# Kernel optimization log

Hardware: AMD Instinct MI355X
Metric: run time of the kernel (lower is better)

Reference implementation:

```python
import jax, jax.numpy as jnp
import numpy as np

NUM_EXPERTS = 32
TOP_K = 4
HIDDEN = 1024
FFN = 2048
BATCH, SEQ = 1, 1024


def setup_inputs() -> dict:
    key = jax.random.key(0)
    ks = jax.random.split(key, 4)
    s = 0.02
    return {
        "x": jax.random.normal(ks[0], (BATCH, SEQ, HIDDEN), jnp.float32),
        "gate_w": jax.random.normal(ks[1], (HIDDEN, NUM_EXPERTS), jnp.float32) * s,
        "gate_b": jnp.zeros((NUM_EXPERTS,), jnp.float32),
        "w1": jax.random.normal(ks[2], (NUM_EXPERTS, HIDDEN, FFN), jnp.float32) * s,
        "b1": jnp.zeros((NUM_EXPERTS, FFN), jnp.float32),
        "w2": jax.random.normal(ks[3], (NUM_EXPERTS, FFN, HIDDEN), jnp.float32) * s,
        "b2": jnp.zeros((NUM_EXPERTS, HIDDEN), jnp.float32),
        "load_ema": jnp.ones((NUM_EXPERTS,), jnp.float32) / NUM_EXPERTS,
        "top_k": TOP_K,
    }


def reference(x, gate_w, gate_b, w1, b1, w2, b2, load_ema, top_k):
    # x: [B, S, d]; eval-mode CompoundMoELayer forward.
    B, S, d = x.shape
    E = gate_w.shape[1]
    flat = x.reshape(-1, d)                              # [N, d]
    N = flat.shape[0]

    # --- router: gate logits -> top-k -> softmax over selected logits ---
    logits = flat @ gate_w + gate_b                      # [N, E]
    top_vals, top_idx = jax.lax.top_k(logits, top_k)     # [N, k]
    weights = jax.nn.softmax(top_vals, axis=-1)          # [N, k]

    # --- switch-style load-balance aux loss ---
    probs = jax.nn.softmax(logits, axis=-1)              # [N, E]
    counts = jax.nn.one_hot(top_idx, E, dtype=flat.dtype).sum(axis=1)  # [N, E]
    frac = counts.mean(axis=0) / top_k                   # [E] routed fraction
    base_aux = E * jnp.sum(frac * probs.mean(axis=0))

    # --- dense combine weights [N, E]: zero for non-selected experts ---
    comb = jnp.zeros((N, E), flat.dtype).at[jnp.arange(N)[:, None], top_idx].add(weights)

    # --- per-expert FFN (GELU, exact erf as torch default), combined ---
    def step(acc, p):
        W1, bb1, W2, bb2, ce = p                         # ce: [N] combine weight
        h = jax.nn.gelu(flat @ W1 + bb1, approximate=False)
        y = h @ W2 + bb2
        return acc + ce[:, None] * y, None

    out, _ = jax.lax.scan(step, jnp.zeros_like(flat), (w1, b1, w2, b2, comb.T))

    # --- compound entropy regularizer over expert load EMA buffer ---
    lp = load_ema / (load_ema.sum() + 1e-8)
    entropy = -jnp.sum(lp * jnp.log(lp + 1e-8))
    reg = jnp.log(jnp.asarray(E, flat.dtype)) - entropy
    aux = base_aux + 0.001 * reg
    return out.reshape(B, S, d), aux
```

## Files before the change

kernel.cpp:

```cpp
#include <hip/hip_runtime.h>
#include <hip/hip_bf16.h>
#include <cmath>

#define N_TOK 1024
#define DIM   1024
#define FFN   2048
#define NE    32
#define TOPK  4
#define TM    256
#define TN    64
#define BK    32
#define BS_STRIDE 40

typedef __attribute__((ext_vector_type(8))) short bf16x8;
typedef __attribute__((ext_vector_type(4))) float f32x4;

#define GLOBAL_AS __attribute__((address_space(1)))
#define LDS_AS    __attribute__((address_space(3)))

__device__ __forceinline__ void g2lds16(const void* g, void* l) {
    __builtin_amdgcn_global_load_lds((const GLOBAL_AS void*)g, (LDS_AS void*)l, 16, 0, 0);
}

__global__ void router_kernel(const float* __restrict__ x, const float* __restrict__ gw,
                              const float* __restrict__ gb, float* __restrict__ probs_mat,
                              int* __restrict__ top_idx, float* __restrict__ top_w) {
    __shared__ float part[8][32];
    __shared__ float logit_s[32];
    int t = threadIdx.x;
    int token = blockIdx.x;
    int e = t & 31, p = t >> 5;
    const float* xr = x + (size_t)token * DIM;
    float acc = 0.f;
    int i0 = p * (DIM / 8);
    for (int i = 0; i < DIM / 8; ++i)
        acc += xr[i0 + i] * gw[(size_t)(i0 + i) * NE + e];
    part[p][e] = acc;
    __syncthreads();
    if (t < 32) {
        float l = gb[t];
        for (int q = 0; q < 8; ++q) l += part[q][t];
        logit_s[t] = l;
    }
    __syncthreads();
    if (t == 0) {
        float l[32];
        for (int i = 0; i < 32; ++i) l[i] = logit_s[i];
        float m = -1e30f;
        for (int i = 0; i < 32; ++i) m = fmaxf(m, l[i]);
        float denom = 0.f;
        for (int i = 0; i < 32; ++i) denom += expf(l[i] - m);
        for (int i = 0; i < 32; ++i)
            probs_mat[(size_t)token * 32 + i] = expf(l[i] - m) / denom;
        float lc[32];
        for (int i = 0; i < 32; ++i) lc[i] = l[i];
        int idx[TOPK]; float val[TOPK];
        for (int k = 0; k < TOPK; ++k) {
            int bj = 0; float bv = lc[0];
            for (int i = 1; i < 32; ++i) if (lc[i] > bv) { bv = lc[i]; bj = i; }
            idx[k] = bj; val[k] = bv; lc[bj] = -1e30f;
        }
        float mm = val[0];
        float w[TOPK]; float ss = 0.f;
        for (int k = 0; k < TOPK; ++k) { w[k] = expf(val[k] - mm); ss += w[k]; }
        for (int k = 0; k < TOPK; ++k) {
            top_idx[token * TOPK + k] = idx[k];
            top_w[token * TOPK + k] = w[k] / ss;
        }
    }
}

__global__ void aux_kernel(const float* __restrict__ probs_mat, const int* __restrict__ top_idx,
                           const float* __restrict__ load_ema, int* __restrict__ counts,
                           int* __restrict__ offsets, int* __restrict__ cursors,
                           float* __restrict__ out_aux) {
    __shared__ int cnt_s[32];
    __shared__ float ps[32];
    __shared__ float psum_part[8][32];
    int t = threadIdx.x;
    if (t < 32) cnt_s[t] = 0;
    __syncthreads();
    for (int i = t; i < N_TOK * TOPK; i += 256) atomicAdd(&cnt_s[top_idx[i]], 1);
    int e = t & 31, p = t >> 5;
    float s = 0.f;
    for (int tok = p; tok < N_TOK; tok += 8) s += probs_mat[(size_t)tok * 32 + e];
    psum_part[p][e] = s;
    __syncthreads();
    if (t < 32) {
        float tot = 0.f;
        for (int q = 0; q < 8; ++q) tot += psum_part[q][t];
        ps[t] = tot;
        counts[t] = cnt_s[t];
    }
    __syncthreads();
    if (t == 0) {
        int off = 0;
        for (int i = 0; i < 32; ++i) { offsets[i] = off; cursors[i] = off; off += cnt_s[i]; }
        offsets[32] = off;
        float base = 0.f;
        for (int i = 0; i < 32; ++i) {
            float frac = (float)cnt_s[i] / (float)(N_TOK * TOPK);
            float mp = ps[i] / (float)N_TOK;
            base += frac * mp;
        }
        base *= (float)NE;
        float sum_ema = 0.f;
        for (int i = 0; i < 32; ++i) sum_ema += load_ema[i];
        float H = 0.f;
        for (int i = 0; i < 32; ++i) {
            float lp = load_ema[i] / (sum_ema + 1e-8f);
            H -= lp * logf(lp + 1e-8f);
        }
        float reg = logf((float)NE) - H;
        *out_aux = base + 0.001f * reg;
    }
}

__global__ void scatter_kernel(const int* __restrict__ top_idx, int* __restrict__ cursors,
                               int* __restrict__ pair_token, int* __restrict__ pair_of) {
    int token = blockIdx.x * 256 + threadIdx.x;
    if (token >= N_TOK) return;
    for (int s = 0; s < TOPK; ++s) {
        int e = top_idx[token * TOPK + s];
        int pos = atomicAdd(&cursors[e], 1);
        pair_token[pos] = token;
        pair_of[token * TOPK + s] = pos;
    }
}

__global__ void convert_x_kernel(const float* __restrict__ x, __hip_bfloat16* __restrict__ xb) {
    int i = (blockIdx.x * 256 + threadIdx.x) * 4;
    float4 v = *(const float4*)&x[i];
    union { __hip_bfloat16 h[4]; ushort4 u; } pk;
    pk.h[0] = __float2bfloat16(v.x);
    pk.h[1] = __float2bfloat16(v.y);
    pk.h[2] = __float2bfloat16(v.z);
    pk.h[3] = __float2bfloat16(v.w);
    *(ushort4*)&xb[i] = pk.u;
}

__global__ __launch_bounds__(256) void gemm1_kernel(
        const __hip_bfloat16* __restrict__ xb, const float* __restrict__ w1,
        const float* __restrict__ b1, const int* __restrict__ offsets,
        const int* __restrict__ pair_token, __hip_bfloat16* __restrict__ h) {
    int e = blockIdx.z;
    int m0 = offsets[e], Me = offsets[e + 1] - m0;
    int rowBase = blockIdx.y * TM;
    if (rowBase >= Me) return;
    int mlim = Me - rowBase; if (mlim > TM) mlim = TM;
    int f0 = blockIdx.x * TN;

    __shared__ __hip_bfloat16 As[TM * BK];
    __shared__ __hip_bfloat16 Bs[TN * BS_STRIDE];
    __shared__ int toks[TM];

    int t = threadIdx.x;
    int w = t >> 6, ln = t & 63;
    int q = ln >> 4, lj = ln & 15;
    { int r = t < mlim ? t : mlim - 1; toks[t] = pair_token[m0 + rowBase + r]; }
    bool act = (w * 64) < mlim;

    int a_sub = ln >> 2, a_part = ln & 3;
    int bn = ln, bkb = w * 8;

    f32x4 acc[4][4] = {};

    for (int k0 = 0; k0 < DIM; k0 += BK) {
        __syncthreads();
        if (act) {
#pragma unroll
            for (int i = 0; i < 4; ++i) {
                int rit = w * 64 + i * 16 + a_sub;
                const __hip_bfloat16* src = xb + (size_t)toks[rit] * DIM + k0 + a_part * 8;
                g2lds16(src, As + (w * 64 + i * 16) * BK);
            }
        }
        {
            const float* bp = w1 + ((size_t)e * DIM + k0 + bkb) * FFN + f0 + bn;
            float bv[8];
#pragma unroll
            for (int j = 0; j < 8; ++j) bv[j] = bp[(size_t)j * FFN];
            union { __hip_bfloat16 hb[8]; int4 v; } u;
#pragma unroll
            for (int j = 0; j < 8; ++j) u.hb[j] = __float2bfloat16(bv[j]);
            *(int4*)&Bs[bn * BS_STRIDE + bkb] = u.v;
        }
        __syncthreads();
        if (act) {
            bf16x8 af[4], bf[4];
#pragma unroll
            for (int ms = 0; ms < 4; ++ms)
                af[ms] = *(const bf16x8*)&As[(w * 64 + ms * 16 + lj) * BK + q * 8];
#pragma unroll
            for (int ns = 0; ns < 4; ++ns)
                bf[ns] = *(const bf16x8*)&Bs[(ns * 16 + lj) * BS_STRIDE + q * 8];
#pragma unroll
            for (int ms = 0; ms < 4; ++ms)
#pragma unroll
                for (int ns = 0; ns < 4; ++ns)
                    acc[ms][ns] = __builtin_amdgcn_mfma_f32_16x16x32_bf16(af[ms], bf[ns], acc[ms][ns], 0, 0, 0);
        }
    }
    if (!act) return;
#pragma unroll
    for (int ms = 0; ms < 4; ++ms) {
#pragma unroll
        for (int rr = 0; rr < 4; ++rr) {
            int rit = w * 64 + ms * 16 + q * 4 + rr;
            if (rit >= mlim) continue;
            size_t rowG = (size_t)(m0 + rowBase + rit);
#pragma unroll
            for (int ns = 0; ns < 4; ++ns) {
                int col = f0 + ns * 16 + lj;
                float v = acc[ms][ns][rr] + b1[(size_t)e * FFN + col];
                float g = 0.5f * v * (1.f + erff(v * 0.70710678118654752f));
                h[rowG * FFN + col] = __float2bfloat16(g);
            }
        }
    }
}

__global__ __launch_bounds__(256) void gemm2_kernel(
        const __hip_bfloat16* __restrict__ h, const float* __restrict__ w2,
        const int* __restrict__ offsets, float* __restrict__ y) {
    int e = blockIdx.z;
    int m0 = offsets[e], Me = offsets[e + 1] - m0;
    int rowBase = blockIdx.y * TM;
    if (rowBase >= Me) return;
    int mlim = Me - rowBase; if (mlim > TM) mlim = TM;
    int d0 = blockIdx.x * TN;

    __shared__ __hip_bfloat16 As[TM * BK];
    __shared__ __hip_bfloat16 Bs[TN * BS_STRIDE];

    int t = threadIdx.x;
    int w = t >> 6, ln = t & 63;
    int q = ln >> 4, lj = ln & 15;
    bool act = (w * 64) < mlim;

    int a_sub = ln >> 2, a_part = ln & 3;
    int bn = ln, bkb = w * 8;

    f32x4 acc[4][4] = {};

    for (int k0 = 0; k0 < FFN; k0 += BK) {
        __syncthreads();
        if (act) {
#pragma unroll
            for (int i = 0; i < 4; ++i) {
                int rit = w * 64 + i * 16 + a_sub;
                if (rit >= mlim) rit = mlim - 1;
                const __hip_bfloat16* src = h + (size_t)(m0 + rowBase + rit) * FFN + k0 + a_part * 8;
                g2lds16(src, As + (w * 64 + i * 16) * BK);
            }
        }
        {
            const float* bp = w2 + ((size_t)e * FFN + k0 + bkb) * DIM + d0 + bn;
            float bv[8];
#pragma unroll
            for (int j = 0; j < 8; ++j) bv[j] = bp[(size_t)j * DIM];
            union { __hip_bfloat16 hb[8]; int4 v; } u;
#pragma unroll
            for (int j = 0; j < 8; ++j) u.hb[j] = __float2bfloat16(bv[j]);
            *(int4*)&Bs[bn * BS_STRIDE + bkb] = u.v;
        }
        __syncthreads();
        if (act) {
            bf16x8 af[4], bf[4];
#pragma unroll
            for (int ms = 0; ms < 4; ++ms)
                af[ms] = *(const bf16x8*)&As[(w * 64 + ms * 16 + lj) * BK + q * 8];
#pragma unroll
            for (int ns = 0; ns < 4; ++ns)
                bf[ns] = *(const bf16x8*)&Bs[(ns * 16 + lj) * BS_STRIDE + q * 8];
#pragma unroll
            for (int ms = 0; ms < 4; ++ms)
#pragma unroll
                for (int ns = 0; ns < 4; ++ns)
                    acc[ms][ns] = __builtin_amdgcn_mfma_f32_16x16x32_bf16(af[ms], bf[ns], acc[ms][ns], 0, 0, 0);
        }
    }
    if (!act) return;
#pragma unroll
    for (int ms = 0; ms < 4; ++ms) {
#pragma unroll
        for (int rr = 0; rr < 4; ++rr) {
            int rit = w * 64 + ms * 16 + q * 4 + rr;
            if (rit >= mlim) continue;
            size_t rowG = (size_t)(m0 + rowBase + rit);
#pragma unroll
            for (int ns = 0; ns < 4; ++ns)
                y[rowG * DIM + d0 + ns * 16 + lj] = acc[ms][ns][rr];
        }
    }
}

__global__ void combine_kernel(const float* __restrict__ y, const float* __restrict__ b2,
        const int* __restrict__ top_idx, const float* __restrict__ top_w,
        const int* __restrict__ pair_of, float* __restrict__ out) {
    int token = blockIdx.y;
    int j = blockIdx.x * 256 + threadIdx.x;
    float acc = 0.f;
#pragma unroll
    for (int s = 0; s < TOPK; ++s) {
        int e = top_idx[token * TOPK + s];
        float w = top_w[token * TOPK + s];
        int p = pair_of[token * TOPK + s];
        acc += w * (y[(size_t)p * DIM + j] + b2[(size_t)e * DIM + j]);
    }
    out[(size_t)token * DIM + j] = acc;
}

extern "C" void kernel_launch(void* const* d_in, const int* in_sizes, int n_in,
                              void* d_out, int out_size, void* d_ws, size_t ws_size,
                              hipStream_t stream) {
    const float* x        = (const float*)d_in[0];
    const float* gate_w   = (const float*)d_in[1];
    const float* gate_b   = (const float*)d_in[2];
    const float* w1       = (const float*)d_in[3];
    const float* b1       = (const float*)d_in[4];
    const float* w2       = (const float*)d_in[5];
    const float* b2       = (const float*)d_in[6];
    const float* load_ema = (const float*)d_in[7];
    float* out = (float*)d_out;

    char* base = (char*)d_ws;
    size_t off = 0;
    auto alloc = [&](size_t bytes) {
        void* p = base + off;
        off = (off + bytes + 255) & ~(size_t)255;
        return p;
    };
    float* probs_mat = (float*)alloc(N_TOK * 32 * sizeof(float));
    int*   top_idx   = (int*)  alloc(N_TOK * TOPK * sizeof(int));
    float* top_w     = (float*)alloc(N_TOK * TOPK * sizeof(float));
    int*   counts    = (int*)  alloc(32 * sizeof(int));
    int*   offsets   = (int*)  alloc(33 * sizeof(int));
    int*   cursors   = (int*)  alloc(32 * sizeof(int));
    int*   pair_token= (int*)  alloc(N_TOK * TOPK * sizeof(int));
    int*   pair_of   = (int*)  alloc(N_TOK * TOPK * sizeof(int));
    __hip_bfloat16* xb = (__hip_bfloat16*)alloc((size_t)N_TOK * DIM * sizeof(__hip_bfloat16));
    __hip_bfloat16* h  = (__hip_bfloat16*)alloc((size_t)N_TOK * TOPK * FFN * sizeof(__hip_bfloat16));
    float* y         = (float*)alloc((size_t)N_TOK * TOPK * DIM * sizeof(float));

    router_kernel<<<N_TOK, 256, 0, stream>>>(x, gate_w, gate_b, probs_mat, top_idx, top_w);
    aux_kernel<<<1, 256, 0, stream>>>(probs_mat, top_idx, load_ema, counts, offsets, cursors,
                                      out + (size_t)N_TOK * DIM);
    scatter_kernel<<<(N_TOK + 255) / 256, 256, 0, stream>>>(top_idx, cursors, pair_token, pair_of);
    convert_x_kernel<<<(N_TOK * DIM / 4 + 255) / 256, 256, 0, stream>>>(x, xb);
    {
        dim3 grid(FFN / TN, (N_TOK * 1 + TM - 1) / TM, NE);
        gemm1_kernel<<<grid, 256, 0, stream>>>(xb, w1, b1, offsets, pair_token, h);
    }
    {
        dim3 grid(DIM / TN, (N_TOK * 1 + TM - 1) / TM, NE);
        gemm2_kernel<<<grid, 256, 0, stream>>>(h, w2, offsets, y);
    }
    {
        dim3 grid(DIM / 256, N_TOK);
        combine_kernel<<<grid, 256, 0, stream>>>(y, b2, top_idx, top_w, pair_of, out);
    }
}
```

Before: 759.3 us.

## Loop row tiles inside expert GEMM blocks, split-K gemm2, fuse x convert into router

GEMM blocks now iterate over all row tiles of an expert instead of launching one block per tile, with TM reduced to 192 and a transposed LDS layout for A. gemm2 splits the FFN reduction in two, writing two partial outputs that the combine kernel sums. The bf16 conversion of x is folded into the router, and router softmax/top-k use wave shuffles instead of a single thread. This aims to cut empty blocks, launch count and serial router work, at the cost of per-expert load imbalance and extra y traffic.

```diff
diff --git a/kernel.cpp b/kernel.cpp
--- a/kernel.cpp
+++ b/kernel.cpp
@@ -7,7 +7,7 @@
 #define FFN   2048
 #define NE    32
 #define TOPK  4
-#define TM    256
+#define TM    192
 #define TN    64
 #define BK    32
 #define BS_STRIDE 40
@@ -22,58 +22,66 @@
     __builtin_amdgcn_global_load_lds((const GLOBAL_AS void*)g, (LDS_AS void*)l, 16, 0, 0);
 }
 
-__global__ void router_kernel(const float* __restrict__ x, const float* __restrict__ gw,
-                              const float* __restrict__ gb, float* __restrict__ probs_mat,
-                              int* __restrict__ top_idx, float* __restrict__ top_w) {
+__global__ __launch_bounds__(256) void router_kernel(
+        const float* __restrict__ x, const float* __restrict__ gw,
+        const float* __restrict__ gb, float* __restrict__ probs_mat,
+        int* __restrict__ top_idx, float* __restrict__ top_w,
+        __hip_bfloat16* __restrict__ xb) {
     __shared__ float part[8][32];
     __shared__ float logit_s[32];
     int t = threadIdx.x;
     int token = blockIdx.x;
+    const float* xr = x + (size_t)token * DIM;
+    {
+        float4 v = *(const float4*)&xr[t * 4];
+        union { __hip_bfloat16 h[4]; ushort4 u; } pk;
+        pk.h[0] = __float2bfloat16(v.x); pk.h[1] = __float2bfloat16(v.y);
+        pk.h[2] = __float2bfloat16(v.z); pk.h[3] = __float2bfloat16(v.w);
+        *(ushort4*)&xb[(size_t)token * DIM + t * 4] = pk.u;
+    }
     int e = t & 31, p = t >> 5;
-    const float* xr = x + (size_t)token * DIM;
     float acc = 0.f;
     int i0 = p * (DIM / 8);
     for (int i = 0; i < DIM / 8; ++i)
         acc += xr[i0 + i] * gw[(size_t)(i0 + i) * NE + e];
     part[p][e] = acc;
     __syncthreads();
-    if (t < 32) {
-        float l = gb[t];
-        for (int q = 0; q < 8; ++q) l += part[q][t];
-        logit_s[t] = l;
-    }
-    __syncthreads();
-    if (t == 0) {
-        float l[32];
-        for (int i = 0; i < 32; ++i) l[i] = logit_s[i];
-        float m = -1e30f;
-        for (int i = 0; i < 32; ++i) m = fmaxf(m, l[i]);
-        float denom = 0.f;
-        for (int i = 0; i < 32; ++i) denom += expf(l[i] - m);
-        for (int i = 0; i < 32; ++i)
-            probs_mat[(size_t)token * 32 + i] = expf(l[i] - m) / denom;
-        float lc[32];
-        for (int i = 0; i < 32; ++i) lc[i] = l[i];
-        int idx[TOPK]; float val[TOPK];
-        for (int k = 0; k < TOPK; ++k) {
-            int bj = 0; float bv = lc[0];
-            for (int i = 1; i < 32; ++i) if (lc[i] > bv) { bv = lc[i]; bj = i; }
-            idx[k] = bj; val[k] = bv; lc[bj] = -1e30f;
-        }
-        float mm = val[0];
-        float w[TOPK]; float ss = 0.f;
-        for (int k = 0; k < TOPK; ++k) { w[k] = expf(val[k] - mm); ss += w[k]; }
-        for (int k = 0; k < TOPK; ++k) {
-            top_idx[token * TOPK + k] = idx[k];
-            top_w[token * TOPK + k] = w[k] / ss;
+    if (t < 64) {
+        float l = -3e38f;
+        if (t < 32) {
+            l = gb[t];
+            for (int q = 0; q < 8; ++q) l += part[q][t];
+        }
+        float m = l;
+        for (int off = 32; off >= 1; off >>= 1) m = fmaxf(m, __shfl_xor(m, off, 64));
+        float ex = (t < 32) ? expf(l - m) : 0.f;
+        float den = ex;
+        for (int off = 32; off >= 1; off >>= 1) den += __shfl_xor(den, off, 64);
+        if (t < 32) probs_mat[(size_t)token * 32 + t] = ex / den;
+        float v = l;
+        float vals[TOPK]; int idxs[TOPK];
+        for (int r = 0; r < TOPK; ++r) {
+            float mv = v;
+            for (int off = 32; off >= 1; off >>= 1) mv = fmaxf(mv, __shfl_xor(mv, off, 64));
+            unsigned long long mask = __ballot(v == mv);
+            int idx = __ffsll((unsigned long long)(mask & 0xffffffffull)) - 1;
+            vals[r] = mv; idxs[r] = idx;
+            if (t == idx) v = -3e38f;
+        }
+        if (t == 0) {
+            float w[TOPK]; float ss = 0.f;
+            for (int r = 0; r < TOPK; ++r) { w[r] = expf(vals[r] - vals[0]); ss += w[r]; }
+            for (int r = 0; r < TOPK; ++r) {
+                top_idx[token * TOPK + r] = idxs[r];
+                top_w[token * TOPK + r] = w[r] / ss;
+            }
         }
     }
 }
 
 __global__ void aux_kernel(const float* __restrict__ probs_mat, const int* __restrict__ top_idx,
-                           const float* __restrict__ load_ema, int* __restrict__ counts,
-                           int* __restrict__ offsets, int* __restrict__ cursors,
-                           float* __restrict__ out_aux) {
+                           const float* __restrict__ load_ema, int* __restrict__ offsets,
+                           int* __restrict__ cursors, float* __restrict__ out_aux) {
     __shared__ int cnt_s[32];
     __shared__ float ps[32];
     __shared__ float psum_part[8][32];
@@ -90,7 +98,6 @@
         float tot = 0.f;
         for (int q = 0; q < 8; ++q) tot += psum_part[q][t];
         ps[t] = tot;
-        counts[t] = cnt_s[t];
     }
     __syncthreads();
     if (t == 0) {
@@ -100,8 +107,7 @@
         float base = 0.f;
         for (int i = 0; i < 32; ++i) {
             float frac = (float)cnt_s[i] / (float)(N_TOK * TOPK);
-            float mp = ps[i] / (float)N_TOK;
-            base += frac * mp;
+            base += frac * (ps[i] / (float)N_TOK);
         }
         base *= (float)NE;
         float sum_ema = 0.f;
@@ -111,8 +117,7 @@
             float lp = load_ema[i] / (sum_ema + 1e-8f);
             H -= lp * logf(lp + 1e-8f);
         }
-        float reg = logf((float)NE) - H;
-        *out_aux = base + 0.001f * reg;
+        *out_aux = base + 0.001f * (logf((float)NE) - H);
     }
 }
 
@@ -128,169 +133,141 @@
     }
 }
 
-__global__ void convert_x_kernel(const float* __restrict__ x, __hip_bfloat16* __restrict__ xb) {
-    int i = (blockIdx.x * 256 + threadIdx.x) * 4;
-    float4 v = *(const float4*)&x[i];
-    union { __hip_bfloat16 h[4]; ushort4 u; } pk;
-    pk.h[0] = __float2bfloat16(v.x);
-    pk.h[1] = __float2bfloat16(v.y);
-    pk.h[2] = __float2bfloat16(v.z);
-    pk.h[3] = __float2bfloat16(v.w);
-    *(ushort4*)&xb[i] = pk.u;
-}
-
-__global__ __launch_bounds__(256) void gemm1_kernel(
+__global__ __launch_bounds__(256, 4) void gemm1_kernel(
         const __hip_bfloat16* __restrict__ xb, const float* __restrict__ w1,
         const float* __restrict__ b1, const int* __restrict__ offsets,
         const int* __restrict__ pair_token, __hip_bfloat16* __restrict__ h) {
     int e = blockIdx.z;
     int m0 = offsets[e], Me = offsets[e + 1] - m0;
-    int rowBase = blockIdx.y * TM;
-    if (rowBase >= Me) return;
-    int mlim = Me - rowBase; if (mlim > TM) mlim = TM;
     int f0 = blockIdx.x * TN;
 
-    __shared__ __hip_bfloat16 As[TM * BK];
+    __shared__ short As[4 * TM * 8];
     __shared__ __hip_bfloat16 Bs[TN * BS_STRIDE];
     __shared__ int toks[TM];
 
     int t = threadIdx.x;
     int w = t >> 6, ln = t & 63;
     int q = ln >> 4, lj = ln & 15;
-    { int r = t < mlim ? t : mlim - 1; toks[t] = pair_token[m0 + rowBase + r]; }
-    bool act = (w * 64) < mlim;
-
-    int a_sub = ln >> 2, a_part = ln & 3;
     int bn = ln, bkb = w * 8;
 
-    f32x4 acc[4][4] = {};
-
-    for (int k0 = 0; k0 < DIM; k0 += BK) {
-        __syncthreads();
-        if (act) {
-#pragma unroll
-            for (int i = 0; i < 4; ++i) {
-                int rit = w * 64 + i * 16 + a_sub;
-                const __hip_bfloat16* src = xb + (size_t)toks[rit] * DIM + k0 + a_part * 8;
-                g2lds16(src, As + (w * 64 + i * 16) * BK);
-            }
-        }
-        {
-            const float* bp = w1 + ((size_t)e * DIM + k0 + bkb) * FFN + f0 + bn;
-            float bv[8];
-#pragma unroll
-            for (int j = 0; j < 8; ++j) bv[j] = bp[(size_t)j * FFN];
-            union { __hip_bfloat16 hb[8]; int4 v; } u;
-#pragma unroll
-            for (int j = 0; j < 8; ++j) u.hb[j] = __float2bfloat16(bv[j]);
-            *(int4*)&Bs[bn * BS_STRIDE + bkb] = u.v;
-        }
-        __syncthreads();
-        if (act) {
-            bf16x8 af[4], bf[4];
-#pragma unroll
-            for (int ms = 0; ms < 4; ++ms)
-                af[ms] = *(const bf16x8*)&As[(w * 64 + ms * 16 + lj) * BK + q * 8];
+    float bias[4];
+#pragma unroll
+    for (int ns = 0; ns < 4; ++ns) bias[ns] = b1[(size_t)e * FFN + f0 + ns * 16 + lj];
+
+    for (int mb = 0; mb < Me; mb += TM) {
+        int mlim = Me - mb; if (mlim > TM) mlim = TM;
+        if (t < TM) {
+            int r = t < mlim ? t : mlim - 1;
+            toks[t] = pair_token[m0 + mb + r];
+        }
+        f32x4 acc[3][4] = {};
+        for (int k0 = 0; k0 < DIM; k0 += BK) {
+            __syncthreads();
+#pragma unroll
+            for (int c = 0; c < 3; ++c) {
+                const __hip_bfloat16* src = xb + (size_t)toks[c * 64 + ln] * DIM + k0 + w * 8;
+                g2lds16(src, As + (w * TM + c * 64) * 8);
+            }
+            {
+                const float* bp = w1 + ((size_t)e * DIM + k0 + bkb) * FFN + f0 + bn;
+                union { __hip_bfloat16 hb[8]; int4 v; } u;
+#pragma unroll
+                for (int j = 0; j < 8; ++j) u.hb[j] = __float2bfloat16(bp[(size_t)j * FFN]);
+                *(int4*)&Bs[bn * BS_STRIDE + bkb] = u.v;
+            }
+            __syncthreads();
+            bf16x8 af[3], bf[4];
+#pragma unroll
+            for (int ms = 0; ms < 3; ++ms)
+                af[ms] = *(const bf16x8*)&As[(q * TM + w * 48 + ms * 16 + lj) * 8];
 #pragma unroll
             for (int ns = 0; ns < 4; ++ns)
                 bf[ns] = *(const bf16x8*)&Bs[(ns * 16 + lj) * BS_STRIDE + q * 8];
 #pragma unroll
-            for (int ms = 0; ms < 4; ++ms)
+            for (int ms = 0; ms < 3; ++ms)
 #pragma unroll
                 for (int ns = 0; ns < 4; ++ns)
                     acc[ms][ns] = __builtin_amdgcn_mfma_f32_16x16x32_bf16(af[ms], bf[ns], acc[ms][ns], 0, 0, 0);
         }
-    }
-    if (!act) return;
-#pragma unroll
-    for (int ms = 0; ms < 4; ++ms) {
-#pragma unroll
-        for (int rr = 0; rr < 4; ++rr) {
-            int rit = w * 64 + ms * 16 + q * 4 + rr;
-            if (rit >= mlim) continue;
-            size_t rowG = (size_t)(m0 + rowBase + rit);
-#pragma unroll
-            for (int ns = 0; ns < 4; ++ns) {
-                int col = f0 + ns * 16 + lj;
-                float v = acc[ms][ns][rr] + b1[(size_t)e * FFN + col];
-                float g = 0.5f * v * (1.f + erff(v * 0.70710678118654752f));
-                h[rowG * FFN + col] = __float2bfloat16(g);
-            }
-        }
-    }
-}
-
-__global__ __launch_bounds__(256) void gemm2_kernel(
+#pragma unroll
+        for (int ms = 0; ms < 3; ++ms) {
+#pragma unroll
+            for (int rr = 0; rr < 4; ++rr) {
+                int rit = w * 48 + ms * 16 + q * 4 + rr;
+                if (rit >= mlim) continue;
+                size_t rowG = (size_t)(m0 + mb + rit);
+#pragma unroll
+                for (int ns = 0; ns < 4; ++ns) {
+                    float v = acc[ms][ns][rr] + bias[ns];
+                    float g = 0.5f * v * (1.f + erff(v * 0.70710678118654752f));
+                    h[rowG * FFN + f0 + ns * 16 + lj] = __float2bfloat16(g);
+                }
+            }
+        }
+    }
+}
+
+__global__ __launch_bounds__(256, 4) void gemm2_kernel(
         const __hip_bfloat16* __restrict__ h, const float* __restrict__ w2,
         const int* __restrict__ offsets, float* __restrict__ y) {
     int e = blockIdx.z;
     int m0 = offsets[e], Me = offsets[e + 1] - m0;
-    int rowBase = blockIdx.y * TM;
-    if (rowBase >= Me) return;
-    int mlim = Me - rowBase; if (mlim > TM) mlim = TM;
     int d0 = blockIdx.x * TN;
-
-    __shared__ __hip_bfloat16 As[TM * BK];
+    int kbase = blockIdx.y * (FFN / 2);
+    float* yp = y + (size_t)blockIdx.y * N_TOK * TOPK * DIM;
+
+    __shared__ short As[4 * TM * 8];
     __shared__ __hip_bfloat16 Bs[TN * BS_STRIDE];
 
     int t = threadIdx.x;
     int w = t >> 6, ln = t & 63;
     int q = ln >> 4, lj = ln & 15;
-    bool act = (w * 64) < mlim;
-
-    int a_sub = ln >> 2, a_part = ln & 3;
     int bn = ln, bkb = w * 8;
 
-    f32x4 acc[4][4] = {};
-
-    for (int k0 = 0; k0 < FFN; k0 += BK) {
-        __syncthreads();
-        if (act) {
-#pragma unroll
-            for (int i = 0; i < 4; ++i) {
-                int rit = w * 64 + i * 16 + a_sub;
-                if (rit >= mlim) rit = mlim - 1;
-                const __hip_bfloat16* src = h + (size_t)(m0 + rowBase + rit) * FFN + k0 + a_part * 8;
-                g2lds16(src, As + (w * 64 + i * 16) * BK);
-            }
-        }
-        {
-            const float* bp = w2 + ((size_t)e * FFN + k0 + bkb) * DIM + d0 + bn;
-            float bv[8];
-#pragma unroll
-            for (int j = 0; j < 8; ++j) bv[j] = bp[(size_t)j * DIM];
-            union { __hip_bfloat16 hb[8]; int4 v; } u;
-#pragma unroll
-            for (int j = 0; j < 8; ++j) u.hb[j] = __float2bfloat16(bv[j]);
-            *(int4*)&Bs[bn * BS_STRIDE + bkb] = u.v;
-        }
-        __syncthreads();
-        if (act) {
-            bf16x8 af[4], bf[4];
-#pragma unroll
-            for (int ms = 0; ms < 4; ++ms)
-                af[ms] = *(const bf16x8*)&As[(w * 64 + ms * 16 + lj) * BK + q * 8];
+    for (int mb = 0; mb < Me; mb += TM) {
+        int mlim = Me - mb; if (mlim > TM) mlim = TM;
+        f32x4 acc[3][4] = {};
+        for (int k0 = 0; k0 < FFN / 2; k0 += BK) {
+            __syncthreads();
+#pragma unroll
+            for (int c = 0; c < 3; ++c) {
+                int rit = c * 64 + ln;
+                int r = rit < mlim ? rit : mlim - 1;
+                const __hip_bfloat16* src = h + (size_t)(m0 + mb + r) * FFN + kbase + k0 + w * 8;
+                g2lds16(src, As + (w * TM + c * 64) * 8);
+            }
+            {
+                const float* bp = w2 + ((size_t)e * FFN + kbase + k0 + bkb) * DIM + d0 + bn;
+                union { __hip_bfloat16 hb[8]; int4 v; } u;
+#pragma unroll
+                for (int j = 0; j < 8; ++j) u.hb[j] = __float2bfloat16(bp[(size_t)j * DIM]);
+                *(int4*)&Bs[bn * BS_STRIDE + bkb] = u.v;
+            }
+            __syncthreads();
+            bf16x8 af[3], bf[4];
+#pragma unroll
+            for (int ms = 0; ms < 3; ++ms)
+                af[ms] = *(const bf16x8*)&As[(q * TM + w * 48 + ms * 16 + lj) * 8];
 #pragma unroll
             for (int ns = 0; ns < 4; ++ns)
                 bf[ns] = *(const bf16x8*)&Bs[(ns * 16 + lj) * BS_STRIDE + q * 8];
 #pragma unroll
-            for (int ms = 0; ms < 4; ++ms)
+            for (int ms = 0; ms < 3; ++ms)
 #pragma unroll
                 for (int ns = 0; ns < 4; ++ns)
                     acc[ms][ns] = __builtin_amdgcn_mfma_f32_16x16x32_bf16(af[ms], bf[ns], acc[ms][ns], 0, 0, 0);
         }
-    }
-    if (!act) return;
-#pragma unroll
-    for (int ms = 0; ms < 4; ++ms) {
-#pragma unroll
-        for (int rr = 0; rr < 4; ++rr) {
-            int rit = w * 64 + ms * 16 + q * 4 + rr;
-            if (rit >= mlim) continue;
-            size_t rowG = (size_t)(m0 + rowBase + rit);
-#pragma unroll
-            for (int ns = 0; ns < 4; ++ns)
-                y[rowG * DIM + d0 + ns * 16 + lj] = acc[ms][ns][rr];
+#pragma unroll
+        for (int ms = 0; ms < 3; ++ms) {
+#pragma unroll
+            for (int rr = 0; rr < 4; ++rr) {
+                int rit = w * 48 + ms * 16 + q * 4 + rr;
+                if (rit >= mlim) continue;
+                size_t rowG = (size_t)(m0 + mb + rit);
+#pragma unroll
+                for (int ns = 0; ns < 4; ++ns)
+                    yp[rowG * DIM + d0 + ns * 16 + lj] = acc[ms][ns][rr];
+            }
         }
     }
 }
@@ -298,6 +275,7 @@
 __global__ void combine_kernel(const float* __restrict__ y, const float* __restrict__ b2,
         const int* __restrict__ top_idx, const float* __restrict__ top_w,
         const int* __restrict__ pair_of, float* __restrict__ out) {
+    const float* y1 = y + (size_t)N_TOK * TOPK * DIM;
     int token = blockIdx.y;
     int j = blockIdx.x * 256 + threadIdx.x;
     float acc = 0.f;
@@ -306,7 +284,7 @@
         int e = top_idx[token * TOPK + s];
         float w = top_w[token * TOPK + s];
         int p = pair_of[token * TOPK + s];
-        acc += w * (y[(size_t)p * DIM + j] + b2[(size_t)e * DIM + j]);
+        acc += w * (y[(size_t)p * DIM + j] + y1[(size_t)p * DIM + j] + b2[(size_t)e * DIM + j]);
     }
     out[(size_t)token * DIM + j] = acc;
 }
@@ -334,26 +312,24 @@
     float* probs_mat = (float*)alloc(N_TOK * 32 * sizeof(float));
     int*   top_idx   = (int*)  alloc(N_TOK * TOPK * sizeof(int));
     float* top_w     = (float*)alloc(N_TOK * TOPK * sizeof(float));
-    int*   counts    = (int*)  alloc(32 * sizeof(int));
     int*   offsets   = (int*)  alloc(33 * sizeof(int));
     int*   cursors   = (int*)  alloc(32 * sizeof(int));
     int*   pair_token= (int*)  alloc(N_TOK * TOPK * sizeof(int));
     int*   pair_of   = (int*)  alloc(N_TOK * TOPK * sizeof(int));
     __hip_bfloat16* xb = (__hip_bfloat16*)alloc((size_t)N_TOK * DIM * sizeof(__hip_bfloat16));
     __hip_bfloat16* h  = (__hip_bfloat16*)alloc((size_t)N_TOK * TOPK * FFN * sizeof(__hip_bfloat16));
-    float* y         = (float*)alloc((size_t)N_TOK * TOPK * DIM * sizeof(float));
-
-    router_kernel<<<N_TOK, 256, 0, stream>>>(x, gate_w, gate_b, probs_mat, top_idx, top_w);
-    aux_kernel<<<1, 256, 0, stream>>>(probs_mat, top_idx, load_ema, counts, offsets, cursors,
+    float* y         = (float*)alloc((size_t)2 * N_TOK * TOPK * DIM * sizeof(float));
+
+    router_kernel<<<N_TOK, 256, 0, stream>>>(x, gate_w, gate_b, probs_mat, top_idx, top_w, xb);
+    aux_kernel<<<1, 256, 0, stream>>>(probs_mat, top_idx, load_ema, offsets, cursors,
                                       out + (size_t)N_TOK * DIM);
     scatter_kernel<<<(N_TOK + 255) / 256, 256, 0, stream>>>(top_idx, cursors, pair_token, pair_of);
-    convert_x_kernel<<<(N_TOK * DIM / 4 + 255) / 256, 256, 0, stream>>>(x, xb);
     {
-        dim3 grid(FFN / TN, (N_TOK * 1 + TM - 1) / TM, NE);
+        dim3 grid(FFN / TN, 1, NE);
         gemm1_kernel<<<grid, 256, 0, stream>>>(xb, w1, b1, offsets, pair_token, h);
     }
     {
-        dim3 grid(DIM / TN, (N_TOK * 1 + TM - 1) / TM, NE);
+        dim3 grid(DIM / TN, 2, NE);
         gemm2_kernel<<<grid, 256, 0, stream>>>(h, w2, offsets, y);
     }
     {
```

New measurement: 664.1 us. -12.5%, faster.
